# Kernel optimization log

Hardware: AMD Instinct MI355X
Metric: run time of the kernel (lower is better)

## Reference

```python
import jax, jax.numpy as jnp
import numpy as np

N = 4096
DIM = 128      # dim_in
HID = 256      # mlp hidden_dim
K_IN = 8       # k for linear_k

def _knn_edges(dist, k):
    # dist: [n,n]; k nearest neighbors excluding self (matches heapq loop)
    n = dist.shape[0]
    d = jnp.where(jnp.eye(n, dtype=bool), jnp.inf, dist)
    nbr = jax.lax.top_k(-d, k)[1]                     # [n,k] indices of k smallest
    src = jnp.repeat(jnp.arange(n), k)                # res[0] = i
    dst = nbr.reshape(-1)                             # res[1] = neighbor
    return src, dst

def _gcn_conv(x, src, dst, W, b):
    # torch_geometric GCNConv: add self loops + symmetric normalization
    n = x.shape[0]
    loop = jnp.arange(n)
    s = jnp.concatenate([src, loop])
    t = jnp.concatenate([dst, loop])
    xw = x @ W
    deg = jax.ops.segment_sum(jnp.ones(s.shape[0], x.dtype), t, num_segments=n)
    dinv = jax.lax.rsqrt(deg)                         # deg >= 1 due to self loops
    norm = dinv[s] * dinv[t]
    out = jax.ops.segment_sum(norm[:, None] * xw[s], t, num_segments=n)
    return out + b

def _gcn(x, src, dst, Wg1, bg1, Wg2, bg2):
    h = jax.nn.relu(_gcn_conv(x, src, dst, Wg1, bg1))
    h = _gcn_conv(h, src, dst, Wg2, bg2)              # dropout is identity in eval
    return jax.nn.log_softmax(h, axis=1)

def _conv2d(x, w, b):
    y = jax.lax.conv_general_dilated(x, w, (1, 1), 'SAME',
        dimension_numbers=('NCHW', 'OIHW', 'NCHW'))
    return y + b.reshape(1, -1, 1, 1)

def setup_inputs():
    key = jax.random.key(0)
    ks = jax.random.split(key, 20)
    f32 = jnp.float32
    def w(k, shape):
        fan = shape[0]
        return (jax.random.uniform(k, shape, f32) * 2 - 1) * (1.0 / np.sqrt(fan))
    return {
        'data_x_1': jax.random.normal(ks[0], (1, N, 4), f32),
        'data_x_2': jax.random.normal(ks[1], (1, N, K_IN, 4), f32),
        'Wk': w(ks[2], (K_IN, 1)),        'bk': jnp.zeros((1,), f32),
        'Wg1': w(ks[3], (8, DIM // 2)),   'bg1': jnp.zeros((DIM // 2,), f32),
        'Wg2': w(ks[4], (DIM // 2, DIM)), 'bg2': jnp.zeros((DIM,), f32),
        'Wq': w(ks[5], (3 * DIM, DIM)),   'bq': jnp.zeros((DIM,), f32),
        'Wkey': w(ks[6], (3 * DIM, DIM)), 'bkey': jnp.zeros((DIM,), f32),
        'Woff': w(ks[7], (4, DIM)),       'boff': jnp.zeros((DIM,), f32),
        'pw': jnp.full((1,), 0.25, f32),
        'Wf1': w(ks[8], (DIM, HID)),      'bf1': jnp.zeros((HID,), f32),
        'Wf2': w(ks[9], (HID, HID)),      'bf2': jnp.zeros((HID,), f32),
        'Wf3': w(ks[10], (HID, 4)),       'bf3': jnp.zeros((4,), f32),
        'Wcy3': w(ks[11], (1, 1, 1, 3)),  'bcy3': jnp.zeros((1,), f32),
        'Wcx3': w(ks[12], (1, 1, 3, 1)),  'bcx3': jnp.zeros((1,), f32),
        'Wcy5': w(ks[13], (1, 1, 1, 5)),  'bcy5': jnp.zeros((1,), f32),
        'Wcx5': w(ks[14], (1, 1, 5, 1)),  'bcx5': jnp.zeros((1,), f32),
        'Wcy9': w(ks[15], (1, 1, 1, 9)),  'bcy9': jnp.zeros((1,), f32),
        'Wcx9': w(ks[16], (1, 1, 9, 1)),  'bcx9': jnp.zeros((1,), f32),
    }

def reference(data_x_1, data_x_2, Wk, bk, Wg1, bg1, Wg2, bg2, Wq, bq, Wkey, bkey,
              Woff, boff, pw, Wf1, bf1, Wf2, bf2, Wf3, bf3,
              Wcy3, bcy3, Wcx3, bcx3, Wcy5, bcy5, Wcx5, bcx5, Wcy9, bcy9, Wcx9, bcx9):
    # linear_k over k dimension: [1,n,k,4] -> transpose -> [1,n,4,k] -> [1,n,4]
    dx2 = jnp.swapaxes(data_x_2, 2, 3)
    dx2_out = (dx2 @ Wk + bk)[..., 0]
    data_x = jnp.concatenate([data_x_1, dx2_out], axis=2)   # [1,n,8]
    Ot = data_x[:, :, 4:]                                   # [1,n,4]

    pos = data_x[:, :, 0:2]
    diff = pos[:, :, None, :] - pos[:, None, :, :]          # [1,n,n,2]
    distances = jnp.linalg.norm(diff, axis=3)               # [1,n,n]
    maxd = jnp.max(distances, axis=2, keepdims=True)
    oushi_atte = 1.0 - distances / maxd                     # [1,n,n]

    x0 = data_x[0]
    dist0 = jax.lax.stop_gradient(distances[0])             # knn on detached dist
    embs = []
    for kk in (3, 5, 9):
        src, dst = _knn_edges(dist0, kk)
        embs.append(_gcn(x0, src, dst, Wg1, bg1, Wg2, bg2)[None])
    embedding = jnp.concatenate(embs, axis=2)               # [1,n,3*DIM]

    query = embedding @ Wq + bq                             # [1,n,DIM]
    key_t = embedding @ Wkey + bkey
    scores = jnp.einsum('bnd,bmd->bnm', query, key_t) / jnp.sqrt(jnp.float32(DIM))
    A = scores / jnp.max(scores, axis=2, keepdims=True)     # [1,n,n]

    A4 = A[None]                                            # [1,1,n,n]
    c3 = _conv2d(A4, Wcy3, bcy3) + _conv2d(A4, Wcx3, bcx3)
    c5 = _conv2d(A4, Wcy5, bcy5) + _conv2d(A4, Wcx5, bcx5)
    c9 = _conv2d(A4, Wcy9, bcy9) + _conv2d(A4, Wcx9, bcx9)

    A_cat = jnp.concatenate([A, oushi_atte, c3[0], c5[0], c9[0]], axis=2)  # [1,n,5n]
    A_cat = (A_cat - A_cat.min()) / (A_cat.max() - A_cat.min())

    Ot5 = jnp.tile(Ot, (1, 5, 1))                           # [1,5n,4]
    h = jnp.matmul(A_cat, Ot5)                              # [1,n,4]
    h = h @ Woff + boff                                     # [1,n,DIM]
    h = jnp.where(h > 0, h, pw * h)                         # PReLU (scalar weight)
    h = jax.nn.relu(h @ Wf1 + bf1)
    h = jax.nn.relu(h @ Wf2 + bf2)
    return h @ Wf3 + bf3                                    # [1,n,4]
```

## Files before the change

kernel.cpp:

```cpp
#include <hip/hip_runtime.h>
#include <math.h>

#define NN 4096

static __device__ __forceinline__ unsigned enc_f(float f){
    unsigned u = __float_as_uint(f);
    return (u & 0x80000000u) ? ~u : (u | 0x80000000u);
}
static __device__ __forceinline__ float dec_f(unsigned u){
    unsigned b = (u & 0x80000000u) ? (u & 0x7fffffffu) : ~u;
    return __uint_as_float(b);
}

__global__ void k_prep(const float* __restrict__ dx1, const float* __restrict__ dx2,
                       const float* __restrict__ Wk, const float* __restrict__ bk,
                       float* __restrict__ x0, float* __restrict__ colsum){
    int n = blockIdx.x*blockDim.x + threadIdx.x;
    if (n >= NN) return;
    float wk[8];
    #pragma unroll
    for (int j=0;j<8;j++) wk[j] = Wk[j];
    float bkv = bk[0];
    #pragma unroll
    for (int c=0;c<4;c++) x0[n*8+c] = dx1[n*4+c];
    #pragma unroll
    for (int c=0;c<4;c++){
        float acc = bkv;
        #pragma unroll
        for (int j=0;j<8;j++) acc += dx2[(n*8+j)*4+c]*wk[j];
        x0[n*8+4+c] = acc;
        atomicAdd(&colsum[c], acc);
    }
}

__global__ void k_ty(const float* __restrict__ x0,
        const float* __restrict__ Wcy3, const float* __restrict__ Wcy5, const float* __restrict__ Wcy9,
        float* __restrict__ Ty){
    int j = blockIdx.x*256 + threadIdx.x;
    if (j >= NN) return;
    float Cy[9];
    #pragma unroll
    for (int o=-4;o<=4;o++){
        float c = Wcy9[o+4];
        if (o>=-2 && o<=2) c += Wcy5[o+2];
        if (o>=-1 && o<=1) c += Wcy3[o+1];
        Cy[o+4] = c;
    }
    float4 acc = {0,0,0,0};
    #pragma unroll
    for (int o=-4;o<=4;o++){
        int jj = j - o;
        if ((unsigned)jj < NN){
            float4 ot = *(const float4*)&x0[jj*8+4];
            float c = Cy[o+4];
            acc.x += c*ot.x; acc.y += c*ot.y; acc.z += c*ot.z; acc.w += c*ot.w;
        }
    }
    *(float4*)&Ty[j*4] = acc;
}

__global__ __launch_bounds__(256) void k_dist(const float* __restrict__ dx1,
        const float* __restrict__ x0,
        float* __restrict__ maxd, int* __restrict__ nbr,
        int* __restrict__ cnt3, int* __restrict__ cnt5, int* __restrict__ cnt9,
        float* __restrict__ dOt){
    __shared__ float2 ps[NN];
    int tid = threadIdx.x;
    for (int j=tid; j<NN; j+=256){
        float4 v = *(const float4*)&dx1[j*4];
        ps[j] = make_float2(v.x, v.y);
    }
    __syncthreads();
    int lane = tid & 63;
    int i = blockIdx.x*4 + (tid>>6);
    float2 pi = ps[i];
    unsigned long long best[9];
    #pragma unroll
    for (int q=0;q<9;q++) best[q] = ~0ULL;
    float lmax = 0.f;
    float4 dacc = {0,0,0,0};
    for (int t=0;t<64;t++){
        int j = (t<<6) | lane;
        float2 p = ps[j];
        float dx = pi.x - p.x, dy = pi.y - p.y;
        float d = sqrtf(dx*dx + dy*dy);
        lmax = fmaxf(lmax, d);
        float4 otj = *(const float4*)&x0[j*8+4];
        dacc.x += d*otj.x; dacc.y += d*otj.y; dacc.z += d*otj.z; dacc.w += d*otj.w;
        unsigned long long cand = ((unsigned long long)__float_as_uint(d) << 32) | (unsigned)j;
        if (j != i && cand < best[8]){
            best[8] = cand;
            #pragma unroll
            for (int q=8; q>0; --q){
                if (best[q] < best[q-1]){ unsigned long long tm=best[q]; best[q]=best[q-1]; best[q-1]=tm; }
            }
        }
    }
    #pragma unroll
    for (int m=1;m<64;m<<=1){
        lmax = fmaxf(lmax, __shfl_xor(lmax, m, 64));
        dacc.x += __shfl_xor(dacc.x, m, 64);
        dacc.y += __shfl_xor(dacc.y, m, 64);
        dacc.z += __shfl_xor(dacc.z, m, 64);
        dacc.w += __shfl_xor(dacc.w, m, 64);
    }
    if (lane==0){
        maxd[i] = lmax;
        *(float4*)&dOt[i*4] = dacc;
    }
    for (int t=0;t<9;t++){
        unsigned long long w = best[0];
        #pragma unroll
        for (int m=1;m<64;m<<=1){
            unsigned long long o = __shfl_xor(w, m, 64);
            if (o < w) w = o;
        }
        if (best[0] == w){
            #pragma unroll
            for (int q=0;q<8;q++) best[q] = best[q+1];
            best[8] = ~0ULL;
        }
        if (lane==0){
            int j = (int)(w & 0xffffffffu);
            nbr[i*9+t] = j;
            atomicAdd(&cnt9[j], 1);
            if (t<5) atomicAdd(&cnt5[j], 1);
            if (t<3) atomicAdd(&cnt3[j], 1);
        }
    }
}

__global__ __launch_bounds__(256) void k_scan(const int* __restrict__ cnt3,
        const int* __restrict__ cnt5, const int* __restrict__ cnt9,
        int* __restrict__ offc, float* __restrict__ dinvc){
    __shared__ int part[256];
    int tid = threadIdx.x;
    for (int g=0; g<3; g++){
        const int* cp = g==0?cnt3:(g==1?cnt5:cnt9);
        int base = tid*16;
        int loc[16]; int s=0;
        #pragma unroll
        for (int q=0;q<16;q++){ loc[q]=s; s += cp[base+q]; }
        part[tid]=s; __syncthreads();
        for (int d=1; d<256; d<<=1){
            int v = (tid>=d) ? part[tid-d] : 0;
            __syncthreads();
            part[tid] += v;
            __syncthreads();
        }
        int pre = (tid==0) ? 0 : part[tid-1];
        #pragma unroll
        for (int q=0;q<16;q++){
            offc[g*NN + base + q]  = pre + loc[q];
            dinvc[g*NN + base + q] = rsqrtf((float)cp[base+q] + 1.f);
        }
        __syncthreads();
    }
}

__global__ void k_fill(const int* __restrict__ nbr, const int* __restrict__ offc,
        int* __restrict__ cur, int* __restrict__ rev){
    int i = blockIdx.x*256 + threadIdx.x;
    if (i >= NN) return;
    #pragma unroll
    for (int t=0;t<9;t++){
        int j = nbr[i*9+t];
        int gmin = t<3 ? 0 : (t<5 ? 1 : 2);
        for (int g=gmin; g<3; g++){
            int pos = atomicAdd(&cur[g*NN+j], 1);
            int rb = (g==0) ? 0 : (g==1 ? NN*3 : NN*8);
            rev[rb + offc[g*NN+j] + pos] = i;
        }
    }
}

__global__ void k_y1(const float* __restrict__ x0, const float* __restrict__ Wg1,
                     float* __restrict__ xw){
    int idx = blockIdx.x*256 + threadIdx.x;
    if (idx >= NN*64) return;
    int n = idx>>6, c = idx&63;
    float acc = 0.f;
    #pragma unroll
    for (int k=0;k<8;k++) acc += x0[n*8+k]*Wg1[k*64+c];
    xw[idx] = acc;
}

__global__ __launch_bounds__(256) void k_h1y2(const float* __restrict__ xw,
        const int* __restrict__ offc,
        const int* __restrict__ cnt3, const int* __restrict__ cnt5, const int* __restrict__ cnt9,
        const int* __restrict__ rev, const float* __restrict__ dinvc,
        const float* __restrict__ bg1, const float* __restrict__ Wg2,
        float* __restrict__ y2){
    __shared__ float h1s[12][64];
    int n0 = blockIdx.x*4, tid = threadIdx.x;
    for (int s=tid; s<768; s+=256){
        int p = s>>6, k = s&63, g = p>>2, n = n0+(p&3);
        const int* cp = g==0?cnt3:(g==1?cnt5:cnt9);
        int rb = (g==0) ? 0 : (g==1 ? NN*3 : NN*8);
        int cnt = cp[n];
        int o = rb + offc[g*NN+n];
        float dv = dinvc[g*NN+n];
        float srow = dv*xw[n*64+k];
        for (int e=0;e<cnt;e++){
            int i = rev[o+e];
            srow += dinvc[g*NN+i]*xw[i*64+k];
        }
        float v = dv*srow + bg1[k];
        h1s[p][k] = v>0.f ? v : 0.f;
    }
    __syncthreads();
    int c = tid & 127, ph = tid>>7;
    float a6[6] = {0,0,0,0,0,0};
    for (int k=0;k<64;k++){
        float w = Wg2[k*128+c];
        #pragma unroll
        for (int q=0;q<6;q++) a6[q] += h1s[q*2+ph][k]*w;
    }
    #pragma unroll
    for (int q=0;q<6;q++){
        int p = q*2+ph, g = p>>2, n = n0+(p&3);
        float dv = dinvc[g*NN+n];
        y2[(size_t)g*NN*128 + (size_t)n*128 + c] = dv*a6[q];
    }
}

__global__ __launch_bounds__(128) void k_fin(const float* __restrict__ y2,
        const int* __restrict__ offc,
        const int* __restrict__ cnt3, const int* __restrict__ cnt5, const int* __restrict__ cnt9,
        const int* __restrict__ rev, const float* __restrict__ dinvc,
        const float* __restrict__ bg2, float* __restrict__ emb){
    __shared__ float sm[2], ss[2];
    int b = blockIdx.x;
    int n = b & (NN-1), g = b >> 12;
    const int* cp = g==0?cnt3:(g==1?cnt5:cnt9);
    int rb = (g==0) ? 0 : (g==1 ? NN*3 : NN*8);
    int cnt = cp[n];
    int o = rb + offc[g*NN+n];
    float dv = dinvc[g*NN+n];
    int c = threadIdx.x;
    const float* yg = y2 + (size_t)g*NN*128;
    float s = yg[(size_t)n*128 + c];
    for (int e=0;e<cnt;e++){
        int i = rev[o+e];
        s += yg[(size_t)i*128 + c];
    }
    float v = dv*s + bg2[c];
    float m = v;
    #pragma unroll
    for (int st=1;st<64;st<<=1) m = fmaxf(m, __shfl_xor(m, st, 64));
    if ((c&63)==0) sm[c>>6] = m;
    __syncthreads();
    m = fmaxf(sm[0], sm[1]);
    float e = expf(v - m);
    float t = e;
    #pragma unroll
    for (int st=1;st<64;st<<=1) t += __shfl_xor(t, st, 64);
    if ((c&63)==0) ss[c>>6] = t;
    __syncthreads();
    t = ss[0]+ss[1];
    emb[n*384 + g*128 + c] = v - m - logf(t);
}

__global__ __launch_bounds__(256) void k_qk(const float* __restrict__ emb,
        const float* __restrict__ Wq, const float* __restrict__ bq,
        const float* __restrict__ Wkey, const float* __restrict__ bkey,
        float* __restrict__ q, float* __restrict__ kbuf){
    __shared__ float es[8][384];
    int n0 = blockIdx.x*8;
    int tid = threadIdx.x;
    for (int idx=tid; idx<8*384; idx+=256){
        int m = idx/384, k = idx%384;
        es[m][k] = emb[(n0+m)*384+k];
    }
    __syncthreads();
    int c = tid & 127;
    int sel = tid >> 7;
    const float* W = sel ? Wkey : Wq;
    float b = sel ? bkey[c] : bq[c];
    float acc[8];
    #pragma unroll
    for (int m=0;m<8;m++) acc[m]=b;
    for (int k=0;k<384;k++){
        float w = W[k*128+c];
        #pragma unroll
        for (int m=0;m<8;m++) acc[m] += es[m][k]*w;
    }
    float* out = sel ? kbuf : q;
    #pragma unroll
    for (int m=0;m<8;m++) out[(n0+m)*128+c] = acc[m];
}

__global__ __launch_bounds__(256) void k_scores(const float* __restrict__ q,
        const float* __restrict__ kb, float* __restrict__ scores,
        unsigned* __restrict__ rowmaxenc, unsigned* __restrict__ rowminenc){
    __shared__ float at[32][132];
    __shared__ float bt[32][132];
    int bx = blockIdx.x & 31;
    int by = blockIdx.x >> 5;
    int r0 = by*128, c0 = bx*128;
    int tid = threadIdx.x;
    int tx = tid & 15, ty = tid >> 4;
    float acc[8][8] = {};
    for (int k0 = 0; k0 < 128; k0 += 32){
        __syncthreads();
        #pragma unroll
        for (int l=0; l<4; l++){
            int idx = tid + l*256;
            int rowi = idx >> 3;
            int kq  = (idx & 7) * 4;
            float4 a = *(const float4*)&q [(size_t)(r0+rowi)*128 + k0 + kq];
            float4 b = *(const float4*)&kb[(size_t)(c0+rowi)*128 + k0 + kq];
            at[kq+0][rowi]=a.x; at[kq+1][rowi]=a.y; at[kq+2][rowi]=a.z; at[kq+3][rowi]=a.w;
            bt[kq+0][rowi]=b.x; bt[kq+1][rowi]=b.y; bt[kq+2][rowi]=b.z; bt[kq+3][rowi]=b.w;
        }
        __syncthreads();
        #pragma unroll
        for (int k=0;k<32;k++){
            float4 a0 = *(const float4*)&at[k][ty*4];
            float4 a1 = *(const float4*)&at[k][64+ty*4];
            float4 b0 = *(const float4*)&bt[k][tx*4];
            float4 b1 = *(const float4*)&bt[k][64+tx*4];
            float av[8] = {a0.x,a0.y,a0.z,a0.w,a1.x,a1.y,a1.z,a1.w};
            float bv[8] = {b0.x,b0.y,b0.z,b0.w,b1.x,b1.y,b1.z,b1.w};
            #pragma unroll
            for (int u=0;u<8;u++){
                #pragma unroll
                for (int v=0;v<8;v++) acc[u][v] += av[u]*bv[v];
            }
        }
    }
    #pragma unroll
    for (int u=0;u<8;u++){
        int rr = r0 + ((u<4)? ty*4+u : 64+ty*4+(u-4));
        float4 s0 = {acc[u][0],acc[u][1],acc[u][2],acc[u][3]};
        float4 s1 = {acc[u][4],acc[u][5],acc[u][6],acc[u][7]};
        *(float4*)&scores[(size_t)rr*NN + c0 + tx*4] = s0;
        *(float4*)&scores[(size_t)rr*NN + c0 + 64 + tx*4] = s1;
        float m = acc[u][0], mn = acc[u][0];
        #pragma unroll
        for (int v=1;v<8;v++){ m = fmaxf(m, acc[u][v]); mn = fminf(mn, acc[u][v]); }
        #pragma unroll
        for (int s=1;s<16;s<<=1){
            m  = fmaxf(m,  __shfl_xor(m,  s, 64));
            mn = fminf(mn, __shfl_xor(mn, s, 64));
        }
        if (tx==0){
            atomicMax(&rowmaxenc[rr], enc_f(m));
            atomicMin(&rowminenc[rr], enc_f(mn));
        }
    }
}

__global__ void k_invr(const unsigned* __restrict__ rowmaxenc, const float* __restrict__ maxd,
        float* __restrict__ invr, float* __restrict__ im){
    int i = blockIdx.x*256 + threadIdx.x;
    if (i >= NN) return;
    invr[i] = 1.f/dec_f(rowmaxenc[i]);
    im[i]   = 1.f/maxd[i];
}

__global__ __launch_bounds__(256) void k_cstream(const float* __restrict__ scores,
        const float* __restrict__ invr,
        const float* __restrict__ Wcy3, const float* __restrict__ Wcx3,
        const float* __restrict__ Wcy5, const float* __restrict__ Wcx5,
        const float* __restrict__ Wcy9, const float* __restrict__ Wcx9,
        const float* __restrict__ bcy3, const float* __restrict__ bcx3,
        const float* __restrict__ bcy5, const float* __restrict__ bcx5,
        const float* __restrict__ bcy9, const float* __restrict__ bcx9,
        float* __restrict__ mnmx){
    __shared__ float smn[4], smx[4];
    int tid = threadIdx.x;
    int w = tid >> 6, lane = tid & 63;
    int strip = blockIdx.x*4 + w;
    int jj = strip*56 - 4 + lane;
    bool cvalid = (unsigned)jj < NN;
    bool outLane = (lane >= 4) && (lane < 60) && cvalid;
    int i0 = blockIdx.y*64;

    float wy3[3],wx3[3],wy5[5],wx5[5],wy9[9],wx9[9];
    #pragma unroll
    for (int t=0;t<3;t++){ wy3[t]=Wcy3[t]; wx3[t]=Wcx3[t]; }
    #pragma unroll
    for (int t=0;t<5;t++){ wy5[t]=Wcy5[t]; wx5[t]=Wcx5[t]; }
    #pragma unroll
    for (int t=0;t<9;t++){ wy9[t]=Wcy9[t]; wx9[t]=Wcx9[t]; }
    float bc3 = bcy3[0]+bcx3[0];
    float bc5 = bcy5[0]+bcx5[0];
    float bc9 = bcy9[0]+bcx9[0];

    float win[9], cy3r[9], cy5r[9], cy9r[9];
    float mn = INFINITY, mx = -INFINITY;

    for (int tb = 0; tb < 8; ++tb){
        #pragma unroll
        for (int u = 0; u < 9; ++u){
            int t  = tb*9 + u;
            int ri = i0 - 4 + t;
            float a = 0.f;
            if (((unsigned)ri < NN) && cvalid)
                a = scores[(size_t)ri*NN + jj] * invr[ri];
            float tp[9];
            #pragma unroll
            for (int k=0;k<9;k++) tp[k] = (k==4) ? a : __shfl(a, lane + k - 4, 64);
            float cy9v = ((tp[0]*wy9[0] + tp[1]*wy9[1]) + (tp[2]*wy9[2] + tp[3]*wy9[3]))
                       + ((tp[4]*wy9[4] + tp[5]*wy9[5]) + (tp[6]*wy9[6] + tp[7]*wy9[7]))
                       + tp[8]*wy9[8];
            float cy5v = ((tp[2]*wy5[0] + tp[3]*wy5[1]) + (tp[4]*wy5[2] + tp[5]*wy5[3]))
                       + tp[6]*wy5[4];
            float cy3v = (tp[3]*wy3[0] + tp[4]*wy3[1]) + tp[5]*wy3[2];
            win[u]  = a;
            cy3r[u] = cy3v; cy5r[u] = cy5v; cy9r[u] = cy9v;
            if (t >= 8 && outLane){
                float cx9v = ((win[(u+1)%9]*wx9[0] + win[(u+2)%9]*wx9[1]) + (win[(u+3)%9]*wx9[2] + win[(u+4)%9]*wx9[3]))
                           + ((win[(u+5)%9]*wx9[4] + win[(u+6)%9]*wx9[5]) + (win[(u+7)%9]*wx9[6] + win[(u+8)%9]*wx9[7]))
                           + win[u]*wx9[8];
                float cx5v = ((win[(u+3)%9]*wx5[0] + win[(u+4)%9]*wx5[1]) + (win[(u+5)%9]*wx5[2] + win[(u+6)%9]*wx5[3]))
                           + win[(u+7)%9]*wx5[4];
                float cx3v = (win[(u+4)%9]*wx3[0] + win[(u+5)%9]*wx3[1]) + win[(u+6)%9]*wx3[2];
                float c9 = cy9r[(u+5)%9] + cx9v + bc9;
                float c5 = cy5r[(u+5)%9] + cx5v + bc5;
                float c3 = cy3r[(u+5)%9] + cx3v + bc3;
                mn = fminf(mn, fminf(fminf(c3,c5),c9));
                mx = fmaxf(mx, fmaxf(fmaxf(c3,c5),c9));
            }
        }
    }
    #pragma unroll
    for (int m=1; m<64; m<<=1){
        mn = fminf(mn, __shfl_xor(mn, m, 64));
        mx = fmaxf(mx, __shfl_xor(mx, m, 64));
    }
    if (lane == 0){ smn[w] = mn; smx[w] = mx; }
    __syncthreads();
    if (tid == 0){
        float a0 = fminf(fminf(smn[0],smn[1]), fminf(smn[2],smn[3]));
        float b0 = fmaxf(fmaxf(smx[0],smx[1]), fmaxf(smx[2],smx[3]));
        int bid = blockIdx.y*gridDim.x + blockIdx.x;
        mnmx[bid] = a0;
        mnmx[1216 + bid] = b0;
    }
}

__global__ __launch_bounds__(256) void k_rowdot(const float* __restrict__ scores,
        const float* __restrict__ x0, const float* __restrict__ Ty,
        const float* __restrict__ invr, const float* __restrict__ im,
        const float* __restrict__ dOt, const float* __restrict__ colsum,
        const float* __restrict__ bcy3, const float* __restrict__ bcx3,
        const float* __restrict__ bcy5, const float* __restrict__ bcx5,
        const float* __restrict__ bcy9, const float* __restrict__ bcx9,
        float* __restrict__ ASdot, float* __restrict__ Bv){
    int tid = threadIdx.x;
    int tc = tid & 31, tr = tid >> 5;
    int i = blockIdx.x*8 + tr;
    const float* srow = scores + (size_t)i*NN;
    float4 ss = {0,0,0,0}, st = {0,0,0,0};
    for (int c0 = tc; c0 < NN; c0 += 32){
        float sv = srow[c0];
        float4 ot = *(const float4*)&x0[c0*8+4];
        float4 ty = *(const float4*)&Ty[c0*4];
        ss.x += sv*ot.x; ss.y += sv*ot.y; ss.z += sv*ot.z; ss.w += sv*ot.w;
        st.x += sv*ty.x; st.y += sv*ty.y; st.z += sv*ty.z; st.w += sv*ty.w;
    }
    #pragma unroll
    for (int s=1; s<32; s<<=1){
        ss.x += __shfl_xor(ss.x, s, 64); ss.y += __shfl_xor(ss.y, s, 64);
        ss.z += __shfl_xor(ss.z, s, 64); ss.w += __shfl_xor(ss.w, s, 64);
        st.x += __shfl_xor(st.x, s, 64); st.y += __shfl_xor(st.y, s, 64);
        st.z += __shfl_xor(st.z, s, 64); st.w += __shfl_xor(st.w, s, 64);
    }
    if (tc == 0){
        float iv = invr[i], imv = im[i];
        float bcsum = bcy3[0]+bcx3[0]+bcy5[0]+bcx5[0]+bcy9[0]+bcx9[0];
        float4 cs = *(const float4*)colsum;
        float4 dv = *(const float4*)&dOt[i*4];
        float4 as;
        as.x = iv*ss.x; as.y = iv*ss.y; as.z = iv*ss.z; as.w = iv*ss.w;
        float k = 1.f + bcsum;
        float4 b;
        b.x = cs.x*k - imv*dv.x + iv*st.x;
        b.y = cs.y*k - imv*dv.y + iv*st.y;
        b.z = cs.z*k - imv*dv.z + iv*st.z;
        b.w = cs.w*k - imv*dv.w + iv*st.w;
        *(float4*)&ASdot[i*4] = as;
        *(float4*)&Bv[i*4]   = b;
    }
}

__global__ __launch_bounds__(256) void k_gmm(const float* __restrict__ mnmx,
        const unsigned* __restrict__ rowminenc, const unsigned* __restrict__ rowmaxenc,
        float* __restrict__ gmm){
    __shared__ float smn[256], smx[256];
    int tid = threadIdx.x;
    float mn = 0.f, mx = 1.f;
    for (int i=tid; i<NN; i+=256){
        float rmx = dec_f(rowmaxenc[i]);
        float q = dec_f(rowminenc[i]) / rmx;
        mn = fminf(mn, fminf(1.f, q));
        mx = fmaxf(mx, fmaxf(1.f, q));
    }
    for (int b=tid; b<1216; b+=256){
        mn = fminf(mn, mnmx[b]);
        mx = fmaxf(mx, mnmx[1216+b]);
    }
    smn[tid]=mn; smx[tid]=mx; __syncthreads();
    for (int s=128;s>0;s>>=1){
        if (tid<s){ smn[tid]=fminf(smn[tid],smn[tid+s]); smx[tid]=fmaxf(smx[tid],smx[tid+s]); }
        __syncthreads();
    }
    if (tid==0){ gmm[0]=smn[0]; gmm[1]=smx[0]; }
}

__global__ void k_hfin(const float* __restrict__ ASdot, const float* __restrict__ Bv,
        const float* __restrict__ Wcx3, const float* __restrict__ Wcx5, const float* __restrict__ Wcx9,
        const float* __restrict__ gmm, const float* __restrict__ colsum,
        float* __restrict__ hfin){
    int i = blockIdx.x*256 + threadIdx.x;
    if (i >= NN) return;
    float Cx[9];
    #pragma unroll
    for (int o=-4;o<=4;o++){
        float c = Wcx9[o+4];
        if (o>=-2 && o<=2) c += Wcx5[o+2];
        if (o>=-1 && o<=1) c += Wcx3[o+1];
        Cx[o+4] = c;
    }
    float4 h = *(const float4*)&Bv[i*4];
    float4 a0 = *(const float4*)&ASdot[i*4];
    h.x += a0.x; h.y += a0.y; h.z += a0.z; h.w += a0.w;
    #pragma unroll
    for (int o=-4;o<=4;o++){
        int r = i + o;
        if ((unsigned)r < NN){
            float4 av = *(const float4*)&ASdot[r*4];
            float c = Cx[o+4];
            h.x += c*av.x; h.y += c*av.y; h.z += c*av.z; h.w += c*av.w;
        }
    }
    float mnv = gmm[0], mxv = gmm[1];
    float s = 1.f/(mxv-mnv), oa = -mnv*s;
    float4 cs = *(const float4*)colsum;
    float4 out;
    out.x = s*h.x + 5.f*oa*cs.x;
    out.y = s*h.y + 5.f*oa*cs.y;
    out.z = s*h.z + 5.f*oa*cs.z;
    out.w = s*h.w + 5.f*oa*cs.w;
    *(float4*)&hfin[i*4] = out;
}

__global__ __launch_bounds__(256) void k_mlp(const float* __restrict__ hfin,
        const float* __restrict__ Woff, const float* __restrict__ boff, const float* __restrict__ pw,
        const float* __restrict__ Wf1, const float* __restrict__ bf1,
        const float* __restrict__ Wf2, const float* __restrict__ bf2,
        const float* __restrict__ Wf3, const float* __restrict__ bf3,
        float* __restrict__ out){
    __shared__ float h1[8][128];
    __shared__ float h2[8][256];
    __shared__ float h3[8][256];
    __shared__ float4 red4[256];
    int n0 = blockIdx.x*8, tid = threadIdx.x;
    float p = pw[0];
    {
        int c = tid & 127, mb = (tid>>7)*4;
        #pragma unroll
        for (int mm=0; mm<4; mm++){
            int m = mb+mm;
            float v = boff[c];
            #pragma unroll
            for (int k=0;k<4;k++) v += hfin[(n0+m)*4+k]*Woff[k*128+c];
            h1[m][c] = v>0.f ? v : p*v;
        }
    }
    __syncthreads();
    {
        int c = tid;
        float acc[8];
        #pragma unroll
        for (int m=0;m<8;m++) acc[m] = bf1[c];
        for (int k=0;k<128;k++){
            float w = Wf1[k*256+c];
            #pragma unroll
            for (int m=0;m<8;m++) acc[m] += h1[m][k]*w;
        }
        #pragma unroll
        for (int m=0;m<8;m++) h2[m][c] = acc[m]>0.f?acc[m]:0.f;
    }
    __syncthreads();
    {
        int c = tid;
        float acc[8];
        #pragma unroll
        for (int m=0;m<8;m++) acc[m] = bf2[c];
        for (int k=0;k<256;k++){
            float w = Wf2[k*256+c];
            #pragma unroll
            for (int m=0;m<8;m++) acc[m] += h2[m][k]*w;
        }
        #pragma unroll
        for (int m=0;m<8;m++) h3[m][c] = acc[m]>0.f?acc[m]:0.f;
    }
    __syncthreads();
    float w3_0 = Wf3[tid*4+0], w3_1 = Wf3[tid*4+1], w3_2 = Wf3[tid*4+2], w3_3 = Wf3[tid*4+3];
    for (int m=0;m<8;m++){
        float hv = h3[m][tid];
        float4 r; r.x = hv*w3_0; r.y = hv*w3_1; r.z = hv*w3_2; r.w = hv*w3_3;
        red4[tid]=r; __syncthreads();
        for (int s=128;s>0;s>>=1){
            if(tid<s){
                red4[tid].x+=red4[tid+s].x; red4[tid].y+=red4[tid+s].y;
                red4[tid].z+=red4[tid+s].z; red4[tid].w+=red4[tid+s].w;
            }
            __syncthreads();
        }
        if (tid==0){
            float4 o;
            o.x = red4[0].x + bf3[0]; o.y = red4[0].y + bf3[1];
            o.z = red4[0].z + bf3[2]; o.w = red4[0].w + bf3[3];
            *(float4*)&out[(n0+m)*4] = o;
        }
        __syncthreads();
    }
}

extern "C" void kernel_launch(void* const* d_in, const int* in_sizes, int n_in,
                              void* d_out, int out_size, void* d_ws, size_t ws_size,
                              hipStream_t stream){
    const float* dx1  = (const float*)d_in[0];
    const float* dx2  = (const float*)d_in[1];
    const float* Wk   = (const float*)d_in[2];
    const float* bk   = (const float*)d_in[3];
    const float* Wg1  = (const float*)d_in[4];
    const float* bg1  = (const float*)d_in[5];
    const float* Wg2  = (const float*)d_in[6];
    const float* bg2  = (const float*)d_in[7];
    const float* Wq   = (const float*)d_in[8];
    const float* bq   = (const float*)d_in[9];
    const float* Wkey = (const float*)d_in[10];
    const float* bkey = (const float*)d_in[11];
    const float* Woff = (const float*)d_in[12];
    const float* boff = (const float*)d_in[13];
    const float* pw   = (const float*)d_in[14];
    const float* Wf1  = (const float*)d_in[15];
    const float* bf1  = (const float*)d_in[16];
    const float* Wf2  = (const float*)d_in[17];
    const float* bf2  = (const float*)d_in[18];
    const float* Wf3  = (const float*)d_in[19];
    const float* bf3  = (const float*)d_in[20];
    const float* Wcy3 = (const float*)d_in[21];
    const float* bcy3 = (const float*)d_in[22];
    const float* Wcx3 = (const float*)d_in[23];
    const float* bcx3 = (const float*)d_in[24];
    const float* Wcy5 = (const float*)d_in[25];
    const float* bcy5 = (const float*)d_in[26];
    const float* Wcx5 = (const float*)d_in[27];
    const float* bcx5 = (const float*)d_in[28];
    const float* Wcy9 = (const float*)d_in[29];
    const float* bcy9 = (const float*)d_in[30];
    const float* Wcx9 = (const float*)d_in[31];
    const float* bcx9 = (const float*)d_in[32];

    char* ws = (char*)d_ws;
    size_t off = 0;
    auto alloc = [&](size_t b)->void*{ void* p = ws + off; off += (b + 255) & ~(size_t)255; return p; };

    char* zbase = ws + off;
    float*    colsum    = (float*)   alloc(4*4);
    int*      cnt3      = (int*)     alloc((size_t)NN*4);
    int*      cnt5      = (int*)     alloc((size_t)NN*4);
    int*      cnt9      = (int*)     alloc((size_t)NN*4);
    int*      cur       = (int*)     alloc((size_t)3*NN*4);
    unsigned* rowmaxenc = (unsigned*)alloc((size_t)NN*4);
    size_t zbytes = (size_t)((ws + off) - zbase);
    unsigned* rowminenc = (unsigned*)alloc((size_t)NN*4);

    float* x0     = (float*)alloc((size_t)NN*8*4);
    float* maxd   = (float*)alloc((size_t)NN*4);
    int*   nbr    = (int*)  alloc((size_t)NN*9*4);
    int*   offc   = (int*)  alloc((size_t)3*NN*4);
    float* dinvc  = (float*)alloc((size_t)3*NN*4);
    int*   rev    = (int*)  alloc((size_t)NN*17*4);
    float* xw     = (float*)alloc((size_t)NN*64*4);
    float* y2     = (float*)alloc((size_t)3*NN*128*4);
    float* emb    = (float*)alloc((size_t)NN*384*4);
    float* qb     = (float*)alloc((size_t)NN*128*4);
    float* kb     = (float*)alloc((size_t)NN*128*4);
    float* scores = (float*)alloc((size_t)NN*NN*4);
    float* Tyb    = (float*)alloc((size_t)NN*4*4);
    float* invr   = (float*)alloc((size_t)NN*4);
    float* im     = (float*)alloc((size_t)NN*4);
    float* dOt    = (float*)alloc((size_t)NN*4*4);
    float* ASd    = (float*)alloc((size_t)NN*4*4);
    float* Bv     = (float*)alloc((size_t)NN*4*4);
    float* mnmx   = (float*)alloc((size_t)2*1216*4);
    float* gmm    = (float*)alloc(2*4);
    float* hfin   = (float*)alloc((size_t)NN*4*4);
    (void)ws_size; (void)in_sizes; (void)n_in; (void)out_size;

    hipMemsetAsync(zbase, 0, zbytes, stream);
    hipMemsetAsync(rowminenc, 0xFF, (size_t)NN*4, stream);

    k_prep<<<16,256,0,stream>>>(dx1,dx2,Wk,bk,x0,colsum);
    k_ty  <<<16,256,0,stream>>>(x0,Wcy3,Wcy5,Wcy9,Tyb);
    k_dist<<<NN/4,256,0,stream>>>(dx1,x0,maxd,nbr,cnt3,cnt5,cnt9,dOt);
    k_scan<<<1,256,0,stream>>>(cnt3,cnt5,cnt9,offc,dinvc);
    k_fill<<<16,256,0,stream>>>(nbr,offc,cur,rev);

    k_y1  <<<NN*64/256,256,0,stream>>>(x0,Wg1,xw);
    k_h1y2<<<NN/4,256,0,stream>>>(xw,offc,cnt3,cnt5,cnt9,rev,dinvc,bg1,Wg2,y2);
    k_fin <<<NN*3,128,0,stream>>>(y2,offc,cnt3,cnt5,cnt9,rev,dinvc,bg2,emb);

    k_qk<<<NN/8,256,0,stream>>>(emb,Wq,bq,Wkey,bkey,qb,kb);
    k_scores<<<1024,256,0,stream>>>(qb,kb,scores,rowmaxenc,rowminenc);
    k_invr<<<16,256,0,stream>>>(rowmaxenc,maxd,invr,im);

    k_cstream<<<dim3(19,64),256,0,stream>>>(scores,invr,
        Wcy3,Wcx3,Wcy5,Wcx5,Wcy9,Wcx9,
        bcy3,bcx3,bcy5,bcx5,bcy9,bcx9, mnmx);
    k_rowdot<<<NN/8,256,0,stream>>>(scores,x0,Tyb,invr,im,dOt,colsum,
        bcy3,bcx3,bcy5,bcx5,bcy9,bcx9, ASd, Bv);
    k_gmm<<<1,256,0,stream>>>(mnmx,rowminenc,rowmaxenc,gmm);
    k_hfin<<<16,256,0,stream>>>(ASd,Bv,Wcx3,Wcx5,Wcx9,gmm,colsum,hfin);
    k_mlp<<<NN/8,256,0,stream>>>(hfin,Woff,boff,pw,Wf1,bf1,Wf2,bf2,Wf3,bf3,(float*)d_out);
}
```

Before: 353.2 us.

## Compute QK^T scores with split-bf16 MFMA and drop the invr kernel

The q and key projections are now written as bf16 high/low pairs, and the 4096x4096 score GEMM uses MFMA 16x16x32 bf16 instructions with three products (hh, hl, lh) to approximate fp32 accuracy. Operands are loaded straight from global memory into registers, with no LDS staging. The separate k_invr kernel is removed, and the consumers decode the row max reciprocal inline. This replaces FP32 FMA work with matrix-core throughput and saves one launch, at the cost of slightly reduced precision and uncoalesced scalar score stores.

```diff
diff --git a/kernel.cpp b/kernel.cpp
--- a/kernel.cpp
+++ b/kernel.cpp
@@ -2,6 +2,9 @@
 #include <math.h>
 
 #define NN 4096
+
+typedef __bf16 bf16x8 __attribute__((ext_vector_type(8)));
+typedef float  f32x4  __attribute__((ext_vector_type(4)));
 
 static __device__ __forceinline__ unsigned enc_f(float f){
     unsigned u = __float_as_uint(f);
@@ -264,7 +267,8 @@
 __global__ __launch_bounds__(256) void k_qk(const float* __restrict__ emb,
         const float* __restrict__ Wq, const float* __restrict__ bq,
         const float* __restrict__ Wkey, const float* __restrict__ bkey,
-        float* __restrict__ q, float* __restrict__ kbuf){
+        __bf16* __restrict__ qh, __bf16* __restrict__ ql,
+        __bf16* __restrict__ kh, __bf16* __restrict__ kl){
     __shared__ float es[8][384];
     int n0 = blockIdx.x*8;
     int tid = threadIdx.x;
@@ -285,82 +289,79 @@
         #pragma unroll
         for (int m=0;m<8;m++) acc[m] += es[m][k]*w;
     }
-    float* out = sel ? kbuf : q;
-    #pragma unroll
-    for (int m=0;m<8;m++) out[(n0+m)*128+c] = acc[m];
-}
-
-__global__ __launch_bounds__(256) void k_scores(const float* __restrict__ q,
-        const float* __restrict__ kb, float* __restrict__ scores,
+    __bf16* oh = sel ? kh : qh;
+    __bf16* ol = sel ? kl : ql;
+    #pragma unroll
+    for (int m=0;m<8;m++){
+        float v = acc[m];
+        __bf16 h = (__bf16)v;
+        oh[(size_t)(n0+m)*128+c] = h;
+        ol[(size_t)(n0+m)*128+c] = (__bf16)(v - (float)h);
+    }
+}
+
+__global__ __launch_bounds__(256) void k_scores(
+        const __bf16* __restrict__ qh, const __bf16* __restrict__ ql,
+        const __bf16* __restrict__ kh, const __bf16* __restrict__ kl,
+        float* __restrict__ scores,
         unsigned* __restrict__ rowmaxenc, unsigned* __restrict__ rowminenc){
-    __shared__ float at[32][132];
-    __shared__ float bt[32][132];
     int bx = blockIdx.x & 31;
     int by = blockIdx.x >> 5;
-    int r0 = by*128, c0 = bx*128;
     int tid = threadIdx.x;
-    int tx = tid & 15, ty = tid >> 4;
-    float acc[8][8] = {};
-    for (int k0 = 0; k0 < 128; k0 += 32){
-        __syncthreads();
-        #pragma unroll
-        for (int l=0; l<4; l++){
-            int idx = tid + l*256;
-            int rowi = idx >> 3;
-            int kq  = (idx & 7) * 4;
-            float4 a = *(const float4*)&q [(size_t)(r0+rowi)*128 + k0 + kq];
-            float4 b = *(const float4*)&kb[(size_t)(c0+rowi)*128 + k0 + kq];
-            at[kq+0][rowi]=a.x; at[kq+1][rowi]=a.y; at[kq+2][rowi]=a.z; at[kq+3][rowi]=a.w;
-            bt[kq+0][rowi]=b.x; bt[kq+1][rowi]=b.y; bt[kq+2][rowi]=b.z; bt[kq+3][rowi]=b.w;
-        }
-        __syncthreads();
-        #pragma unroll
-        for (int k=0;k<32;k++){
-            float4 a0 = *(const float4*)&at[k][ty*4];
-            float4 a1 = *(const float4*)&at[k][64+ty*4];
-            float4 b0 = *(const float4*)&bt[k][tx*4];
-            float4 b1 = *(const float4*)&bt[k][64+tx*4];
-            float av[8] = {a0.x,a0.y,a0.z,a0.w,a1.x,a1.y,a1.z,a1.w};
-            float bv[8] = {b0.x,b0.y,b0.z,b0.w,b1.x,b1.y,b1.z,b1.w};
-            #pragma unroll
-            for (int u=0;u<8;u++){
-                #pragma unroll
-                for (int v=0;v<8;v++) acc[u][v] += av[u]*bv[v];
+    int w = tid >> 6, lane = tid & 63;
+    int li = lane & 15, g = lane >> 4;
+    int r0 = by*128 + (w>>1)*64;
+    int c0 = bx*128 + (w&1)*64;
+
+    f32x4 acc[4][4] = {};
+    for (int ks=0; ks<4; ++ks){
+        int kofs = ks*32 + g*8;
+        bf16x8 ah[4], al[4], bh[4], bl[4];
+        #pragma unroll
+        for (int f=0; f<4; ++f){
+            ah[f] = *(const bf16x8*)&qh[(size_t)(r0+f*16+li)*128 + kofs];
+            al[f] = *(const bf16x8*)&ql[(size_t)(r0+f*16+li)*128 + kofs];
+            bh[f] = *(const bf16x8*)&kh[(size_t)(c0+f*16+li)*128 + kofs];
+            bl[f] = *(const bf16x8*)&kl[(size_t)(c0+f*16+li)*128 + kofs];
+        }
+        #pragma unroll
+        for (int fr=0; fr<4; ++fr){
+            #pragma unroll
+            for (int fc=0; fc<4; ++fc){
+                acc[fr][fc] = __builtin_amdgcn_mfma_f32_16x16x32_bf16(ah[fr], bh[fc], acc[fr][fc], 0, 0, 0);
+                acc[fr][fc] = __builtin_amdgcn_mfma_f32_16x16x32_bf16(ah[fr], bl[fc], acc[fr][fc], 0, 0, 0);
+                acc[fr][fc] = __builtin_amdgcn_mfma_f32_16x16x32_bf16(al[fr], bh[fc], acc[fr][fc], 0, 0, 0);
             }
         }
     }
     #pragma unroll
-    for (int u=0;u<8;u++){
-        int rr = r0 + ((u<4)? ty*4+u : 64+ty*4+(u-4));
-        float4 s0 = {acc[u][0],acc[u][1],acc[u][2],acc[u][3]};
-        float4 s1 = {acc[u][4],acc[u][5],acc[u][6],acc[u][7]};
-        *(float4*)&scores[(size_t)rr*NN + c0 + tx*4] = s0;
-        *(float4*)&scores[(size_t)rr*NN + c0 + 64 + tx*4] = s1;
-        float m = acc[u][0], mn = acc[u][0];
-        #pragma unroll
-        for (int v=1;v<8;v++){ m = fmaxf(m, acc[u][v]); mn = fminf(mn, acc[u][v]); }
-        #pragma unroll
-        for (int s=1;s<16;s<<=1){
-            m  = fmaxf(m,  __shfl_xor(m,  s, 64));
-            mn = fminf(mn, __shfl_xor(mn, s, 64));
-        }
-        if (tx==0){
-            atomicMax(&rowmaxenc[rr], enc_f(m));
-            atomicMin(&rowminenc[rr], enc_f(mn));
-        }
-    }
-}
-
-__global__ void k_invr(const unsigned* __restrict__ rowmaxenc, const float* __restrict__ maxd,
-        float* __restrict__ invr, float* __restrict__ im){
-    int i = blockIdx.x*256 + threadIdx.x;
-    if (i >= NN) return;
-    invr[i] = 1.f/dec_f(rowmaxenc[i]);
-    im[i]   = 1.f/maxd[i];
+    for (int fr=0; fr<4; ++fr){
+        #pragma unroll
+        for (int r=0; r<4; ++r){
+            int row = r0 + fr*16 + g*4 + r;
+            float mx = -INFINITY, mn = INFINITY;
+            #pragma unroll
+            for (int fc=0; fc<4; ++fc){
+                float v = acc[fr][fc][r];
+                scores[(size_t)row*NN + c0 + fc*16 + li] = v;
+                mx = fmaxf(mx, v);
+                mn = fminf(mn, v);
+            }
+            #pragma unroll
+            for (int s=1; s<16; s<<=1){
+                mx = fmaxf(mx, __shfl_xor(mx, s, 64));
+                mn = fminf(mn, __shfl_xor(mn, s, 64));
+            }
+            if (li == 0){
+                atomicMax(&rowmaxenc[row], enc_f(mx));
+                atomicMin(&rowminenc[row], enc_f(mn));
+            }
+        }
+    }
 }
 
 __global__ __launch_bounds__(256) void k_cstream(const float* __restrict__ scores,
-        const float* __restrict__ invr,
+        const unsigned* __restrict__ rowmaxenc,
         const float* __restrict__ Wcy3, const float* __restrict__ Wcx3,
         const float* __restrict__ Wcy5, const float* __restrict__ Wcx5,
         const float* __restrict__ Wcy9, const float* __restrict__ Wcx9,
@@ -398,7 +399,7 @@
             int ri = i0 - 4 + t;
             float a = 0.f;
             if (((unsigned)ri < NN) && cvalid)
-                a = scores[(size_t)ri*NN + jj] * invr[ri];
+                a = scores[(size_t)ri*NN + jj] * (1.f/dec_f(rowmaxenc[ri]));
             float tp[9];
             #pragma unroll
             for (int k=0;k<9;k++) tp[k] = (k==4) ? a : __shfl(a, lane + k - 4, 64);
@@ -443,7 +444,7 @@
 
 __global__ __launch_bounds__(256) void k_rowdot(const float* __restrict__ scores,
         const float* __restrict__ x0, const float* __restrict__ Ty,
-        const float* __restrict__ invr, const float* __restrict__ im,
+        const unsigned* __restrict__ rowmaxenc, const float* __restrict__ maxd,
         const float* __restrict__ dOt, const float* __restrict__ colsum,
         const float* __restrict__ bcy3, const float* __restrict__ bcx3,
         const float* __restrict__ bcy5, const float* __restrict__ bcx5,
@@ -469,7 +470,8 @@
         st.z += __shfl_xor(st.z, s, 64); st.w += __shfl_xor(st.w, s, 64);
     }
     if (tc == 0){
-        float iv = invr[i], imv = im[i];
+        float iv = 1.f/dec_f(rowmaxenc[i]);
+        float imv = 1.f/maxd[i];
         float bcsum = bcy3[0]+bcx3[0]+bcy5[0]+bcx5[0]+bcy9[0]+bcx9[0];
         float4 cs = *(const float4*)colsum;
         float4 dv = *(const float4*)&dOt[i*4];
@@ -681,12 +683,12 @@
     float* xw     = (float*)alloc((size_t)NN*64*4);
     float* y2     = (float*)alloc((size_t)3*NN*128*4);
     float* emb    = (float*)alloc((size_t)NN*384*4);
-    float* qb     = (float*)alloc((size_t)NN*128*4);
-    float* kb     = (float*)alloc((size_t)NN*128*4);
+    __bf16* qh   = (__bf16*)alloc((size_t)NN*128*2);
+    __bf16* ql   = (__bf16*)alloc((size_t)NN*128*2);
+    __bf16* kh   = (__bf16*)alloc((size_t)NN*128*2);
+    __bf16* kl   = (__bf16*)alloc((size_t)NN*128*2);
     float* scores = (float*)alloc((size_t)NN*NN*4);
     float* Tyb    = (float*)alloc((size_t)NN*4*4);
-    float* invr   = (float*)alloc((size_t)NN*4);
-    float* im     = (float*)alloc((size_t)NN*4);
     float* dOt    = (float*)alloc((size_t)NN*4*4);
     float* ASd    = (float*)alloc((size_t)NN*4*4);
     float* Bv     = (float*)alloc((size_t)NN*4*4);
@@ -708,14 +710,13 @@
     k_h1y2<<<NN/4,256,0,stream>>>(xw,offc,cnt3,cnt5,cnt9,rev,dinvc,bg1,Wg2,y2);
     k_fin <<<NN*3,128,0,stream>>>(y2,offc,cnt3,cnt5,cnt9,rev,dinvc,bg2,emb);
 
-    k_qk<<<NN/8,256,0,stream>>>(emb,Wq,bq,Wkey,bkey,qb,kb);
-    k_scores<<<1024,256,0,stream>>>(qb,kb,scores,rowmaxenc,rowminenc);
-    k_invr<<<16,256,0,stream>>>(rowmaxenc,maxd,invr,im);
-
-    k_cstream<<<dim3(19,64),256,0,stream>>>(scores,invr,
+    k_qk<<<NN/8,256,0,stream>>>(emb,Wq,bq,Wkey,bkey,qh,ql,kh,kl);
+    k_scores<<<1024,256,0,stream>>>(qh,ql,kh,kl,scores,rowmaxenc,rowminenc);
+
+    k_cstream<<<dim3(19,64),256,0,stream>>>(scores,rowmaxenc,
         Wcy3,Wcx3,Wcy5,Wcx5,Wcy9,Wcx9,
         bcy3,bcx3,bcy5,bcx5,bcy9,bcx9, mnmx);
-    k_rowdot<<<NN/8,256,0,stream>>>(scores,x0,Tyb,invr,im,dOt,colsum,
+    k_rowdot<<<NN/8,256,0,stream>>>(scores,x0,Tyb,rowmaxenc,maxd,dOt,colsum,
         bcy3,bcx3,bcy5,bcx5,bcy9,bcx9, ASd, Bv);
     k_gmm<<<1,256,0,stream>>>(mnmx,rowminenc,rowmaxenc,gmm);
     k_hfin<<<16,256,0,stream>>>(ASd,Bv,Wcx3,Wcx5,Wcx9,gmm,colsum,hfin);
```

Measured after the change: 347.2 us. Within noise of the previous version (-1.7%).
